# Performance work log

Measured on AMD Instinct MI355X. Metric: run time of the kernel, lower is better.

The kernel has to match this reference:

```python
import jax, jax.numpy as jnp
import numpy as np

NEG = -1e9

def _lstm_dir(x, w_ih, w_hh, b_ih, b_hh):
    # x: (N, T, in) -> (N, T, H); torch gate order i, f, g, o
    xi = x @ w_ih.T + (b_ih + b_hh)  # (N, T, 4H) input projection precomputed
    H = w_hh.shape[1]
    h0 = jnp.zeros((x.shape[0], H), x.dtype)
    def step(carry, xt):
        h, c = carry
        g = xt + h @ w_hh.T
        i, f, gg, o = jnp.split(g, 4, axis=-1)
        c = jax.nn.sigmoid(f) * c + jax.nn.sigmoid(i) * jnp.tanh(gg)
        h = jax.nn.sigmoid(o) * jnp.tanh(c)
        return (h, c), h
    _, ys = jax.lax.scan(step, (h0, h0), jnp.swapaxes(xi, 0, 1))
    return jnp.swapaxes(ys, 0, 1)

def _bilstm_layer(x, wif, whf, bif, bhf, wib, whb, bib, bhb):
    fwd = _lstm_dir(x, wif, whf, bif, bhf)
    bwd = _lstm_dir(x[:, ::-1], wib, whb, bib, bhb)[:, ::-1]
    return jnp.concatenate([fwd, bwd], axis=-1)

def _na1d(x, qkv_w, qkv_b, rpb, proj_w, proj_b, heads, kernel):
    # NATTEN-style 1D neighborhood attention with edge-clamped window + rel pos bias.
    N, L, Dm = x.shape
    hd = Dm // heads
    qkv = x @ qkv_w.T + qkv_b
    q, k, v = jnp.split(qkv, 3, axis=-1)
    sh = lambda t: t.reshape(N, L, heads, hd).transpose(0, 2, 1, 3)
    q, k, v = sh(q) * (hd ** -0.5), sh(k), sh(v)
    scores = jnp.einsum('nhid,nhjd->nhij', q, k)  # (N, heads, L, L)
    i = jnp.arange(L)[:, None]
    j = jnp.arange(L)[None, :]
    start = jnp.clip(i - kernel // 2, 0, L - kernel)     # window start per query
    mask = (j >= start) & (j < start + kernel)           # (L, L) neighborhood mask
    rel = jnp.clip(j - i + kernel - 1, 0, 2 * kernel - 2)
    bias = rpb[:, rel]                                   # (heads, L, L)
    scores = jnp.where(mask, scores + bias, NEG)
    attn = jax.nn.softmax(scores, axis=-1)
    out = jnp.einsum('nhij,nhjd->nhid', attn, v)
    out = out.transpose(0, 2, 1, 3).reshape(N, L, Dm)
    return out @ proj_w.T + proj_b

def setup_inputs() -> dict:
    key = jax.random.key(0)
    ks = iter(jax.random.split(key, 40))
    B, IN, T, P, Dm, H = 4, 256, 256, 88, 128, 64
    p = lambda *s: jax.random.normal(next(ks), s, jnp.float32) * 0.05
    inp = {'x': jax.random.normal(next(ks), (B, IN, T, P), jnp.float32)}
    for l, fin in (('l0', IN), ('l1', Dm)):
        for suf in ('', 'r'):
            inp['w_ih_' + l + suf] = p(4 * H, fin)
            inp['w_hh_' + l + suf] = p(4 * H, H)
            inp['b_ih_' + l + suf] = p(4 * H)
            inp['b_hh_' + l + suf] = p(4 * H)
    for tag, kz in (('t', 7), ('f', 87)):
        inp['qkv_w_' + tag] = p(3 * Dm, Dm)
        inp['qkv_b_' + tag] = p(3 * Dm)
        inp['rpb_' + tag] = p(1, 2 * kz - 1)
        inp['proj_w_' + tag] = p(Dm, Dm)
        inp['proj_b_' + tag] = p(Dm)
    return inp

def reference(x, w_ih_l0, w_hh_l0, b_ih_l0, b_hh_l0, w_ih_l0r, w_hh_l0r, b_ih_l0r, b_hh_l0r, w_ih_l1, w_hh_l1, b_ih_l1, b_hh_l1, w_ih_l1r, w_hh_l1r, b_ih_l1r, b_hh_l1r, qkv_w_t, qkv_b_t, rpb_t, proj_w_t, proj_b_t, qkv_w_f, qkv_b_f, rpb_f, proj_w_f, proj_b_f):
    B, IN, T, P = x.shape
    Dm = proj_w_t.shape[0]
    h = jnp.transpose(x, (0, 3, 2, 1)).reshape(B * P, T, IN)
    h = _bilstm_layer(h, w_ih_l0, w_hh_l0, b_ih_l0, b_hh_l0, w_ih_l0r, w_hh_l0r, b_ih_l0r, b_hh_l0r)
    h = _bilstm_layer(h, w_ih_l1, w_hh_l1, b_ih_l1, b_hh_l1, w_ih_l1r, w_hh_l1r, b_ih_l1r, b_hh_l1r)
    h = _na1d(h, qkv_w_t, qkv_b_t, rpb_t, proj_w_t, proj_b_t, 1, 7)            # time axis
    h = h.reshape(B, P, T, Dm).transpose(0, 2, 1, 3).reshape(B * T, P, Dm)
    h = _na1d(h, qkv_w_f, qkv_b_f, rpb_f, proj_w_f, proj_b_f, 1, 87)           # pitch axis
    return h.reshape(B, T, P, Dm)
```

## Files before the change

### kernel.cpp

```cpp
#include <hip/hip_runtime.h>
#include <cstdint>

#define TP 22528
#define MROWS 90112

typedef __bf16 bf16x8 __attribute__((ext_vector_type(8)));
typedef float  f32x4  __attribute__((ext_vector_type(4)));
typedef unsigned short ushort8 __attribute__((ext_vector_type(8)));

__device__ __forceinline__ unsigned short f2bf(float x) {
    unsigned u = __builtin_bit_cast(unsigned, x);
    return (unsigned short)((u + 0x7fffu + ((u >> 16) & 1u)) >> 16);
}
__device__ __forceinline__ float bf2f(unsigned short h) {
    return __builtin_bit_cast(float, (unsigned)h << 16);
}
__device__ __forceinline__ void gl16(const void* g, void* l) {
    __builtin_amdgcn_global_load_lds(
        (const __attribute__((address_space(1))) void*)g,
        (__attribute__((address_space(3))) void*)l, 16, 0, 0);
}

__global__ void convert_w(const float* __restrict__ s0, const float* __restrict__ s1,
                          const float* __restrict__ s2, const float* __restrict__ s3,
                          const float* __restrict__ s4, const float* __restrict__ s5,
                          const float* __restrict__ s6, const float* __restrict__ s7,
                          unsigned short* __restrict__ WH, unsigned short* __restrict__ WL)
{
    const int stride = gridDim.x * blockDim.x;
    for (int i = blockIdx.x * blockDim.x + threadIdx.x; i < 327680; i += stride) {
        const float* s; int base;
        if      (i <  65536) { s = s0; base = 0; }
        else if (i < 131072) { s = s1; base = 65536; }
        else if (i < 163840) { s = s2; base = 131072; }
        else if (i < 196608) { s = s3; base = 163840; }
        else if (i < 245760) { s = s4; base = 196608; }
        else if (i < 262144) { s = s5; base = 245760; }
        else if (i < 311296) { s = s6; base = 262144; }
        else                 { s = s7; base = 311296; }
        const float v = s[i - base];
        const unsigned short h = f2bf(v);
        WH[i] = h; WL[i] = f2bf(v - bf2f(h));
    }
}

__launch_bounds__(256)
__global__ void transpose_x(const float* __restrict__ x,
                            unsigned short* __restrict__ Xh,
                            unsigned short* __restrict__ Xl)
{
    __shared__ float tile[64][65];
    const int tid = threadIdx.x;
    const int tp0 = blockIdx.x * 64, k0 = blockIdx.y * 64, b = blockIdx.z;
    #pragma unroll
    for (int i = 0; i < 16; ++i) {
        const int idx = i * 256 + tid;
        const int kl = idx >> 6, tpl = idx & 63;
        tile[kl][tpl] = x[(size_t)(b * 256 + k0 + kl) * TP + tp0 + tpl];
    }
    __syncthreads();
    #pragma unroll
    for (int i = 0; i < 2; ++i) {
        const int u = i * 2048 + tid * 8;
        const int ml = u >> 6, kl0 = u & 63;
        ushort8 hi, lo;
        #pragma unroll
        for (int j = 0; j < 8; ++j) {
            const float v = tile[kl0 + j][ml];
            const unsigned short h = f2bf(v);
            hi[j] = h; lo[j] = f2bf(v - bf2f(h));
        }
        const size_t row = (size_t)b * TP + tp0 + ml;
        *(ushort8*)&Xh[row * 256 + k0 + kl0] = hi;
        *(ushort8*)&Xl[row * 256 + k0 + kl0] = lo;
    }
}

template<int OUTBF>
__launch_bounds__(256, 2)
__global__ void gemm_bf16(const unsigned short* __restrict__ Ahi,
                          const unsigned short* __restrict__ Alo,
                          const unsigned short* __restrict__ Whi0,
                          const unsigned short* __restrict__ Wlo0,
                          const unsigned short* __restrict__ Whi1,
                          const unsigned short* __restrict__ Wlo1,
                          const float* __restrict__ b0a, const float* __restrict__ b0b,
                          const float* __restrict__ b1a, const float* __restrict__ b1b,
                          float* __restrict__ C,
                          unsigned short* __restrict__ Chi, unsigned short* __restrict__ Clo,
                          int ldc, int K, int splitN, int NB)
{
    __shared__ unsigned short lds[32768];
    const int tid  = threadIdx.x;
    const int bid  = blockIdx.x;
    const int q8   = (int)gridDim.x >> 3;
    const int wq   = (bid & 7) * q8 + (bid >> 3);
    const int nb   = wq % NB;
    const int mb   = wq / NB;
    const int n0   = nb * 128;
    const int m0   = mb * 128;
    const unsigned short* Wh; const unsigned short* Wl;
    const float* ba; const float* bb; int nr0;
    if (n0 < splitN) { Wh = Whi0; Wl = Wlo0; ba = b0a; bb = b0b; nr0 = n0; }
    else             { Wh = Whi1; Wl = Wlo1; ba = b1a; bb = b1b; nr0 = n0 - splitN; }
    const int lane = tid & 63;
    const int wv   = tid >> 6;
    const int wm   = wv >> 1, wn = wv & 1;
    const int lr   = lane & 15, lg = lane >> 4;
    const int voff = (lane >> 2) * K + (((lane & 3) ^ ((lane >> 2) & 3)) * 8);
    const int wb   = wv * 1024;

    const unsigned short* gAh = Ahi + (size_t)(m0 + wv * 32) * K + voff;
    const unsigned short* gAl = Alo + (size_t)(m0 + wv * 32) * K + voff;
    const unsigned short* gBh = Wh + (size_t)(nr0 + wv * 32) * K + voff;
    const unsigned short* gBl = Wl + (size_t)(nr0 + wv * 32) * K + voff;

    const int NT = K >> 5;
    f32x4 acc[4][4] = {};

    auto stage = [&](int bufi, int ks) {
        unsigned short* base = lds + bufi * 16384;
        gl16(gAh + ks,          base +         wb);
        gl16(gAh + ks + 16 * K, base +         wb + 512);
        gl16(gAl + ks,          base + 4096  + wb);
        gl16(gAl + ks + 16 * K, base + 4096  + wb + 512);
        gl16(gBh + ks,          base + 8192  + wb);
        gl16(gBh + ks + 16 * K, base + 8192  + wb + 512);
        gl16(gBl + ks,          base + 12288 + wb);
        gl16(gBl + ks + 16 * K, base + 12288 + wb + 512);
    };

    stage(0, 0);
    for (int t = 0; t < NT; ++t) {
        const int cur = (t & 1) * 16384;
        if (t + 1 < NT) {
            stage((t & 1) ^ 1, (t + 1) * 32);
            asm volatile("s_waitcnt vmcnt(8)" ::: "memory");
        } else {
            asm volatile("s_waitcnt vmcnt(0)" ::: "memory");
        }
        __builtin_amdgcn_s_barrier();
        __builtin_amdgcn_sched_barrier(0);
        bf16x8 ah[4], al[4], bh[4], bl[4];
        #pragma unroll
        for (int mf = 0; mf < 4; ++mf) {
            const int r = wm * 64 + mf * 16 + lr;
            const int o = r * 32 + ((lg ^ (r & 3)) * 8);
            ah[mf] = *(const bf16x8*)&lds[cur + o];
            al[mf] = *(const bf16x8*)&lds[cur + 4096 + o];
        }
        #pragma unroll
        for (int nf = 0; nf < 4; ++nf) {
            const int r = wn * 64 + nf * 16 + lr;
            const int o = r * 32 + ((lg ^ (r & 3)) * 8);
            bh[nf] = *(const bf16x8*)&lds[cur + 8192 + o];
            bl[nf] = *(const bf16x8*)&lds[cur + 12288 + o];
        }
        #pragma unroll
        for (int mf = 0; mf < 4; ++mf)
            #pragma unroll
            for (int nf = 0; nf < 4; ++nf) {
                acc[mf][nf] = __builtin_amdgcn_mfma_f32_16x16x32_bf16(ah[mf], bh[nf], acc[mf][nf], 0, 0, 0);
                acc[mf][nf] = __builtin_amdgcn_mfma_f32_16x16x32_bf16(ah[mf], bl[nf], acc[mf][nf], 0, 0, 0);
                acc[mf][nf] = __builtin_amdgcn_mfma_f32_16x16x32_bf16(al[mf], bh[nf], acc[mf][nf], 0, 0, 0);
            }
        __builtin_amdgcn_s_barrier();
        __builtin_amdgcn_sched_barrier(0);
    }
    #pragma unroll
    for (int nf = 0; nf < 4; ++nf) {
        const int ncol = wn * 64 + nf * 16 + lr;
        const float bias = ba[nr0 + ncol] + (bb ? bb[nr0 + ncol] : 0.0f);
        #pragma unroll
        for (int mf = 0; mf < 4; ++mf) {
            const int row = m0 + wm * 64 + mf * 16 + lg * 4;
            #pragma unroll
            for (int i = 0; i < 4; ++i) {
                const float v = acc[mf][nf][i] + bias;
                if (OUTBF) {
                    const size_t o = (size_t)(row + i) * ldc + n0 + ncol;
                    const unsigned short h = f2bf(v);
                    Chi[o] = h; Clo[o] = f2bf(v - bf2f(h));
                } else {
                    C[(size_t)(row + i) * ldc + n0 + ncol] = v;
                }
            }
        }
    }
}

__launch_bounds__(256)
__global__ void lstm_kernel(const float* __restrict__ XI,
                            const float* __restrict__ whh_f,
                            const float* __restrict__ whh_b,
                            unsigned short* __restrict__ Hh,
                            unsigned short* __restrict__ Hl)
{
    const int bid = blockIdx.x;
    const int dir = bid & 1;
    const int n   = bid >> 1;
    const int b   = n / 88, p = n - 88 * (n / 88);
    const int j   = threadIdx.x;
    const float* whh = dir ? whh_b : whh_f;
    const int j0 = dir ? 256 : 0;
    const int ho = dir ? 64 : 0;
    float w[64];
    #pragma unroll
    for (int k = 0; k < 64; k += 4) {
        const float4 wv = *(const float4*)(whh + (size_t)j * 64 + k);
        w[k] = wv.x; w[k+1] = wv.y; w[k+2] = wv.z; w[k+3] = wv.w;
    }
    __shared__ float h_sh[64];
    __shared__ float acts[256];
    if (j < 64) h_sh[j] = 0.0f;
    float c = 0.0f;
    __syncthreads();
    const size_t rowbase = (size_t)(b * 256) * 88 + p;
    float pref = XI[(rowbase + (size_t)(dir ? 255 : 0) * 88) * 512 + j0 + j];
    for (int step = 0; step < 256; ++step) {
        const int t = dir ? (255 - step) : step;
        const size_t r = rowbase + (size_t)t * 88;
        float gs0 = pref, gs1 = 0.0f, gs2 = 0.0f, gs3 = 0.0f;
        if (step + 1 < 256) {
            const int tn = dir ? (254 - step) : (step + 1);
            pref = XI[(rowbase + (size_t)tn * 88) * 512 + j0 + j];
        }
        #pragma unroll
        for (int k = 0; k < 64; k += 16) {
            const float4 h0 = *(const float4*)&h_sh[k];
            const float4 h1 = *(const float4*)&h_sh[k + 4];
            const float4 h2 = *(const float4*)&h_sh[k + 8];
            const float4 h3 = *(const float4*)&h_sh[k + 12];
            gs0 += h0.x * w[k]    + h0.y * w[k+1]  + h0.z * w[k+2]  + h0.w * w[k+3];
            gs1 += h1.x * w[k+4]  + h1.y * w[k+5]  + h1.z * w[k+6]  + h1.w * w[k+7];
            gs2 += h2.x * w[k+8]  + h2.y * w[k+9]  + h2.z * w[k+10] + h2.w * w[k+11];
            gs3 += h3.x * w[k+12] + h3.y * w[k+13] + h3.z * w[k+14] + h3.w * w[k+15];
        }
        const float g = (gs0 + gs1) + (gs2 + gs3);
        float a;
        if (j >= 128 && j < 192) {
            const float e = __expf(2.0f * g);
            a = 1.0f - 2.0f / (e + 1.0f);
        } else {
            a = 1.0f / (1.0f + __expf(-g));
        }
        acts[j] = a;
        __syncthreads();
        if (j < 64) {
            const float ai = acts[j], af = acts[64 + j], ag = acts[128 + j], ao = acts[192 + j];
            c = af * c + ai * ag;
            const float e = __expf(2.0f * c);
            const float th = 1.0f - 2.0f / (e + 1.0f);
            const float h = ao * th;
            h_sh[j] = h;
            const size_t o = r * 128 + ho + j;
            const unsigned short hh = f2bf(h);
            Hh[o] = hh; Hl[o] = f2bf(h - bf2f(hh));
        }
        __syncthreads();
    }
}

__launch_bounds__(256)
__global__ void na_t_kernel(const float* __restrict__ QKV,
                            const float* __restrict__ rpb,
                            unsigned short* __restrict__ OUTh,
                            unsigned short* __restrict__ OUTl)
{
    const int wave = threadIdx.x >> 6;
    const int lane = threadIdx.x & 63;
    const int q = blockIdx.x * 4 + wave;
    const int b = q / TP; int rem = q - b * TP;
    const int i = rem / 88; const int p = rem - 88 * (rem / 88);
    int start = i - 3; if (start < 0) start = 0; if (start > 249) start = 249;
    const float scale = 0.08838834764831845f;
    const float* qrow = QKV + (size_t)q * 384;
    const float q0 = qrow[lane] * scale;
    const float q1 = qrow[lane + 64] * scale;
    const size_t rbase = (size_t)(b * 256) * 88 + p;
    float s[7];
    #pragma unroll
    for (int jj = 0; jj < 7; ++jj) {
        const int t = start + jj;
        const float* krow = QKV + (rbase + (size_t)t * 88) * 384 + 128;
        float part = q0 * krow[lane] + q1 * krow[lane + 64];
        part += __shfl_xor(part, 1);
        part += __shfl_xor(part, 2);
        part += __shfl_xor(part, 4);
        part += __shfl_xor(part, 8);
        part += __shfl_xor(part, 16);
        part += __shfl_xor(part, 32);
        int rel = t - i + 6; if (rel < 0) rel = 0; if (rel > 12) rel = 12;
        s[jj] = part + rpb[rel];
    }
    float m = s[0];
    #pragma unroll
    for (int jj = 1; jj < 7; ++jj) m = fmaxf(m, s[jj]);
    float sum = 0.0f;
    #pragma unroll
    for (int jj = 0; jj < 7; ++jj) { s[jj] = __expf(s[jj] - m); sum += s[jj]; }
    const float inv = 1.0f / sum;
    float o0 = 0.0f, o1 = 0.0f;
    #pragma unroll
    for (int jj = 0; jj < 7; ++jj) {
        const float* vrow = QKV + (rbase + (size_t)(start + jj) * 88) * 384 + 256;
        const float pj = s[jj] * inv;
        o0 += pj * vrow[lane];
        o1 += pj * vrow[lane + 64];
    }
    const size_t oi = (size_t)q * 128 + lane;
    const unsigned short h0 = f2bf(o0);
    OUTh[oi] = h0; OUTl[oi] = f2bf(o0 - bf2f(h0));
    const unsigned short h1 = f2bf(o1);
    OUTh[oi + 64] = h1; OUTl[oi + 64] = f2bf(o1 - bf2f(h1));
}

#define LPAD 133
#define SPAD 89
__launch_bounds__(256)
__global__ void na_f_kernel(const float* __restrict__ QKV,
                            const float* __restrict__ rpb,
                            unsigned short* __restrict__ OUTh,
                            unsigned short* __restrict__ OUTl)
{
    __shared__ float Qs[96][LPAD];
    __shared__ float Ks[96][LPAD];
    __shared__ float Ss[96][SPAD];
    const int blk = blockIdx.x;
    const int tid = threadIdx.x;
    const size_t base = (size_t)blk * 88 * 384;
    const float scale = 0.08838834764831845f;
    for (int f = tid; f < 2816; f += 256) {
        const int row = f >> 5, c4 = (f & 31) * 4;
        const float4 qv = *(const float4*)(QKV + base + (size_t)row * 384 + c4);
        Qs[row][c4+0] = qv.x * scale; Qs[row][c4+1] = qv.y * scale;
        Qs[row][c4+2] = qv.z * scale; Qs[row][c4+3] = qv.w * scale;
        const float4 kv = *(const float4*)(QKV + base + (size_t)row * 384 + 128 + c4);
        Ks[row][c4+0] = kv.x; Ks[row][c4+1] = kv.y;
        Ks[row][c4+2] = kv.z; Ks[row][c4+3] = kv.w;
    }
    __syncthreads();
    const int tx = tid & 15, ty = tid >> 4;
    {
        float acc[6][6] = {};
        for (int kk = 0; kk < 128; ++kk) {
            float a[6], bb[6];
            #pragma unroll
            for (int i = 0; i < 6; ++i) a[i] = Qs[ty*6 + i][kk];
            #pragma unroll
            for (int j = 0; j < 6; ++j) bb[j] = Ks[tx*6 + j][kk];
            #pragma unroll
            for (int i = 0; i < 6; ++i)
                #pragma unroll
                for (int j = 0; j < 6; ++j)
                    acc[i][j] += a[i] * bb[j];
        }
        #pragma unroll
        for (int i = 0; i < 6; ++i) {
            const int qq = ty*6 + i;
            if (qq < 88) {
                #pragma unroll
                for (int j = 0; j < 6; ++j) {
                    const int k = tx*6 + j;
                    if (k < 88) Ss[qq][k] = acc[i][j];
                }
            }
        }
    }
    __syncthreads();
    for (int f = tid; f < 2816; f += 256) {
        const int row = f >> 5, c4 = (f & 31) * 4;
        const float4 vv = *(const float4*)(QKV + base + (size_t)row * 384 + 256 + c4);
        Ks[row][c4+0] = vv.x; Ks[row][c4+1] = vv.y;
        Ks[row][c4+2] = vv.z; Ks[row][c4+3] = vv.w;
    }
    if (tid < 88) {
        const int i = tid;
        const int jex = (i <= 43) ? 87 : 0;
        float m = -1e30f;
        for (int k = 0; k < 88; ++k) {
            if (k == jex) continue;
            int rel = k - i + 86; if (rel < 0) rel = 0; if (rel > 172) rel = 172;
            const float v = Ss[i][k] + rpb[rel];
            Ss[i][k] = v;
            m = fmaxf(m, v);
        }
        float sum = 0.0f;
        for (int k = 0; k < 88; ++k) {
            if (k == jex) continue;
            const float e = __expf(Ss[i][k] - m);
            Ss[i][k] = e;
            sum += e;
        }
        const float inv = 1.0f / sum;
        for (int k = 0; k < 88; ++k) Ss[i][k] = (k == jex) ? 0.0f : Ss[i][k] * inv;
    }
    __syncthreads();
    {
        float o[6][8] = {};
        for (int k = 0; k < 88; ++k) {
            float pv[6], vv[8];
            #pragma unroll
            for (int i = 0; i < 6; ++i) pv[i] = Ss[ty*6 + i][k];
            #pragma unroll
            for (int j = 0; j < 8; ++j) vv[j] = Ks[k][tx + 16*j];
            #pragma unroll
            for (int i = 0; i < 6; ++i)
                #pragma unroll
                for (int j = 0; j < 8; ++j)
                    o[i][j] += pv[i] * vv[j];
        }
        #pragma unroll
        for (int i = 0; i < 6; ++i) {
            const int qq = ty*6 + i;
            if (qq < 88) {
                const size_t ro = ((size_t)blk * 88 + qq) * 128;
                #pragma unroll
                for (int j = 0; j < 8; ++j) {
                    const float v = o[i][j];
                    const unsigned short hh = f2bf(v);
                    OUTh[ro + tx + 16*j] = hh;
                    OUTl[ro + tx + 16*j] = f2bf(v - bf2f(hh));
                }
            }
        }
    }
}

extern "C" void kernel_launch(void* const* d_in, const int* in_sizes, int n_in,
                              void* d_out, int out_size, void* d_ws, size_t ws_size,
                              hipStream_t stream)
{
    const float* x         = (const float*)d_in[0];
    const float* w_ih_l0   = (const float*)d_in[1];
    const float* w_hh_l0   = (const float*)d_in[2];
    const float* b_ih_l0   = (const float*)d_in[3];
    const float* b_hh_l0   = (const float*)d_in[4];
    const float* w_ih_l0r  = (const float*)d_in[5];
    const float* w_hh_l0r  = (const float*)d_in[6];
    const float* b_ih_l0r  = (const float*)d_in[7];
    const float* b_hh_l0r  = (const float*)d_in[8];
    const float* w_ih_l1   = (const float*)d_in[9];
    const float* w_hh_l1   = (const float*)d_in[10];
    const float* b_ih_l1   = (const float*)d_in[11];
    const float* b_hh_l1   = (const float*)d_in[12];
    const float* w_ih_l1r  = (const float*)d_in[13];
    const float* w_hh_l1r  = (const float*)d_in[14];
    const float* b_ih_l1r  = (const float*)d_in[15];
    const float* b_hh_l1r  = (const float*)d_in[16];
    const float* qkv_w_t   = (const float*)d_in[17];
    const float* qkv_b_t   = (const float*)d_in[18];
    const float* rpb_t     = (const float*)d_in[19];
    const float* proj_w_t  = (const float*)d_in[20];
    const float* proj_b_t  = (const float*)d_in[21];
    const float* qkv_w_f   = (const float*)d_in[22];
    const float* qkv_b_f   = (const float*)d_in[23];
    const float* rpb_f     = (const float*)d_in[24];
    const float* proj_w_f  = (const float*)d_in[25];
    const float* proj_b_f  = (const float*)d_in[26];

    float* ws = (float*)d_ws;
    float*          XI   = ws;
    float*          QKV  = ws;
    unsigned short* ATTh = (unsigned short*)(ws + (size_t)MROWS * 384);
    unsigned short* ATTl = ATTh + (size_t)MROWS * 128;
    unsigned short* Hh   = (unsigned short*)(ws + 46137344);
    unsigned short* Hl   = Hh + (size_t)MROWS * 128;
    unsigned short* Gh   = (unsigned short*)(ws + 57671680);
    unsigned short* Gl   = Gh + (size_t)MROWS * 128;
    unsigned short* Xh   = (unsigned short*)(ws + 46137344);
    unsigned short* Xl   = Xh + (size_t)MROWS * 256;
    unsigned short* WH   = (unsigned short*)(ws + 69206016);
    unsigned short* WL   = WH + 327680;

    const int BIG = 1 << 30;
    const dim3 blk(256);

    convert_w<<<dim3(320), blk, 0, stream>>>(w_ih_l0, w_ih_l0r, w_ih_l1, w_ih_l1r,
        qkv_w_t, proj_w_t, qkv_w_f, proj_w_f, WH, WL);
    transpose_x<<<dim3(352, 4, 4), blk, 0, stream>>>(x, Xh, Xl);
    gemm_bf16<0><<<dim3(2816), blk, 0, stream>>>(Xh, Xl,
        WH, WL, WH + 65536, WL + 65536,
        b_ih_l0, b_hh_l0, b_ih_l0r, b_hh_l0r,
        XI, nullptr, nullptr, 512, 256, 256, 4);
    lstm_kernel<<<dim3(704), blk, 0, stream>>>(XI, w_hh_l0, w_hh_l0r, Hh, Hl);
    gemm_bf16<0><<<dim3(2816), blk, 0, stream>>>(Hh, Hl,
        WH + 131072, WL + 131072, WH + 163840, WL + 163840,
        b_ih_l1, b_hh_l1, b_ih_l1r, b_hh_l1r,
        XI, nullptr, nullptr, 512, 128, 256, 4);
    lstm_kernel<<<dim3(704), blk, 0, stream>>>(XI, w_hh_l1, w_hh_l1r, Hh, Hl);
    gemm_bf16<0><<<dim3(2112), blk, 0, stream>>>(Hh, Hl,
        WH + 196608, WL + 196608, WH + 196608, WL + 196608,
        qkv_b_t, nullptr, qkv_b_t, nullptr,
        QKV, nullptr, nullptr, 384, 128, BIG, 3);
    na_t_kernel<<<dim3(22528), blk, 0, stream>>>(QKV, rpb_t, ATTh, ATTl);
    gemm_bf16<1><<<dim3(704), blk, 0, stream>>>(ATTh, ATTl,
        WH + 245760, WL + 245760, WH + 245760, WL + 245760,
        proj_b_t, nullptr, proj_b_t, nullptr,
        nullptr, Gh, Gl, 128, 128, BIG, 1);
    gemm_bf16<0><<<dim3(2112), blk, 0, stream>>>(Gh, Gl,
        WH + 262144, WL + 262144, WH + 262144, WL + 262144,
        qkv_b_f, nullptr, qkv_b_f, nullptr,
        QKV, nullptr, nullptr, 384, 128, BIG, 3);
    na_f_kernel<<<dim3(1024), blk, 0, stream>>>(QKV, rpb_f, ATTh, ATTl);
    gemm_bf16<0><<<dim3(704), blk, 0, stream>>>(ATTh, ATTl,
        WH + 311296, WL + 311296, WH + 311296, WL + 311296,
        proj_b_f, nullptr, proj_b_f, nullptr,
        (float*)d_out, nullptr, nullptr, 128, 128, BIG, 1);
}
```

Before: 1.104 ms.

## Halve LSTM block to 128 threads, each computing two gates in registers

The recurrent LSTM kernel now uses 128 threads per sequence instead of 256. Each thread holds two rows of W_hh: wave 0 computes the i and g gates, wave 1 the f and o gates. Only the i*g product goes through shared memory, so the 256-entry activation array is dropped. This roughly halves the threads waiting at each per-timestep barrier and removes most of the shared-memory traffic on the serial critical path. In exchange, register use per thread doubles to 128 weight floats and each thread does twice the FMA work per step.

```diff
diff --git a/kernel.cpp b/kernel.cpp
--- a/kernel.cpp
+++ b/kernel.cpp
@@ -189,7 +189,7 @@
     }
 }
 
-__launch_bounds__(256)
+__launch_bounds__(128)
 __global__ void lstm_kernel(const float* __restrict__ XI,
                             const float* __restrict__ whh_f,
                             const float* __restrict__ whh_b,
@@ -200,60 +200,69 @@
     const int dir = bid & 1;
     const int n   = bid >> 1;
     const int b   = n / 88, p = n - 88 * (n / 88);
-    const int j   = threadIdx.x;
+    const int tid = threadIdx.x;
+    const int u   = tid & 63;
+    const int wv  = tid >> 6;
     const float* whh = dir ? whh_b : whh_f;
     const int j0 = dir ? 256 : 0;
     const int ho = dir ? 64 : 0;
-    float w[64];
+    const int rowA = wv * 64 + u;
+    const int rowB = 128 + wv * 64 + u;
+    float wA[64], wB[64];
     #pragma unroll
     for (int k = 0; k < 64; k += 4) {
-        const float4 wv = *(const float4*)(whh + (size_t)j * 64 + k);
-        w[k] = wv.x; w[k+1] = wv.y; w[k+2] = wv.z; w[k+3] = wv.w;
+        const float4 wa = *(const float4*)(whh + (size_t)rowA * 64 + k);
+        wA[k] = wa.x; wA[k+1] = wa.y; wA[k+2] = wa.z; wA[k+3] = wa.w;
+        const float4 wb2 = *(const float4*)(whh + (size_t)rowB * 64 + k);
+        wB[k] = wb2.x; wB[k+1] = wb2.y; wB[k+2] = wb2.z; wB[k+3] = wb2.w;
     }
     __shared__ float h_sh[64];
-    __shared__ float acts[256];
-    if (j < 64) h_sh[j] = 0.0f;
+    __shared__ float ig_sh[64];
+    if (tid < 64) h_sh[tid] = 0.0f;
     float c = 0.0f;
     __syncthreads();
     const size_t rowbase = (size_t)(b * 256) * 88 + p;
-    float pref = XI[(rowbase + (size_t)(dir ? 255 : 0) * 88) * 512 + j0 + j];
+    const size_t r0 = rowbase + (size_t)(dir ? 255 : 0) * 88;
+    float prefA = XI[r0 * 512 + j0 + rowA];
+    float prefB = XI[r0 * 512 + j0 + rowB];
     for (int step = 0; step < 256; ++step) {
         const int t = dir ? (255 - step) : step;
         const size_t r = rowbase + (size_t)t * 88;
-        float gs0 = pref, gs1 = 0.0f, gs2 = 0.0f, gs3 = 0.0f;
+        float gA0 = prefA, gA1 = 0.0f, gB0 = prefB, gB1 = 0.0f;
         if (step + 1 < 256) {
             const int tn = dir ? (254 - step) : (step + 1);
-            pref = XI[(rowbase + (size_t)tn * 88) * 512 + j0 + j];
-        }
-        #pragma unroll
-        for (int k = 0; k < 64; k += 16) {
+            const size_t rn = rowbase + (size_t)tn * 88;
+            prefA = XI[rn * 512 + j0 + rowA];
+            prefB = XI[rn * 512 + j0 + rowB];
+        }
+        #pragma unroll
+        for (int k = 0; k < 64; k += 8) {
             const float4 h0 = *(const float4*)&h_sh[k];
             const float4 h1 = *(const float4*)&h_sh[k + 4];
-            const float4 h2 = *(const float4*)&h_sh[k + 8];
-            const float4 h3 = *(const float4*)&h_sh[k + 12];
-            gs0 += h0.x * w[k]    + h0.y * w[k+1]  + h0.z * w[k+2]  + h0.w * w[k+3];
-            gs1 += h1.x * w[k+4]  + h1.y * w[k+5]  + h1.z * w[k+6]  + h1.w * w[k+7];
-            gs2 += h2.x * w[k+8]  + h2.y * w[k+9]  + h2.z * w[k+10] + h2.w * w[k+11];
-            gs3 += h3.x * w[k+12] + h3.y * w[k+13] + h3.z * w[k+14] + h3.w * w[k+15];
-        }
-        const float g = (gs0 + gs1) + (gs2 + gs3);
-        float a;
-        if (j >= 128 && j < 192) {
-            const float e = __expf(2.0f * g);
-            a = 1.0f - 2.0f / (e + 1.0f);
+            gA0 += h0.x * wA[k]   + h0.y * wA[k+1] + h0.z * wA[k+2] + h0.w * wA[k+3];
+            gA1 += h1.x * wA[k+4] + h1.y * wA[k+5] + h1.z * wA[k+6] + h1.w * wA[k+7];
+            gB0 += h0.x * wB[k]   + h0.y * wB[k+1] + h0.z * wB[k+2] + h0.w * wB[k+3];
+            gB1 += h1.x * wB[k+4] + h1.y * wB[k+5] + h1.z * wB[k+6] + h1.w * wB[k+7];
+        }
+        const float gAs = gA0 + gA1;
+        const float gBs = gB0 + gB1;
+        const float aA = 1.0f / (1.0f + __expf(-gAs));
+        float aB;
+        if (wv == 0) {
+            const float e = __expf(2.0f * gBs);
+            aB = 1.0f - 2.0f / (e + 1.0f);
         } else {
-            a = 1.0f / (1.0f + __expf(-g));
-        }
-        acts[j] = a;
+            aB = 1.0f / (1.0f + __expf(-gBs));
+        }
+        if (wv == 0) ig_sh[u] = aA * aB;
         __syncthreads();
-        if (j < 64) {
-            const float ai = acts[j], af = acts[64 + j], ag = acts[128 + j], ao = acts[192 + j];
-            c = af * c + ai * ag;
+        if (wv == 1) {
+            c = aA * c + ig_sh[u];
             const float e = __expf(2.0f * c);
             const float th = 1.0f - 2.0f / (e + 1.0f);
-            const float h = ao * th;
-            h_sh[j] = h;
-            const size_t o = r * 128 + ho + j;
+            const float h = aB * th;
+            h_sh[u] = h;
+            const size_t o = r * 128 + ho + u;
             const unsigned short hh = f2bf(h);
             Hh[o] = hh; Hl[o] = f2bf(h - bf2f(hh));
         }
@@ -483,12 +492,12 @@
         WH, WL, WH + 65536, WL + 65536,
         b_ih_l0, b_hh_l0, b_ih_l0r, b_hh_l0r,
         XI, nullptr, nullptr, 512, 256, 256, 4);
-    lstm_kernel<<<dim3(704), blk, 0, stream>>>(XI, w_hh_l0, w_hh_l0r, Hh, Hl);
+    lstm_kernel<<<dim3(704), dim3(128), 0, stream>>>(XI, w_hh_l0, w_hh_l0r, Hh, Hl);
     gemm_bf16<0><<<dim3(2816), blk, 0, stream>>>(Hh, Hl,
         WH + 131072, WL + 131072, WH + 163840, WL + 163840,
         b_ih_l1, b_hh_l1, b_ih_l1r, b_hh_l1r,
         XI, nullptr, nullptr, 512, 128, 256, 4);
-    lstm_kernel<<<dim3(704), blk, 0, stream>>>(XI, w_hh_l1, w_hh_l1r, Hh, Hl);
+    lstm_kernel<<<dim3(704), dim3(128), 0, stream>>>(XI, w_hh_l1, w_hh_l1r, Hh, Hl);
     gemm_bf16<0><<<dim3(2112), blk, 0, stream>>>(Hh, Hl,
         WH + 196608, WL + 196608, WH + 196608, WL + 196608,
         qkv_b_t, nullptr, qkv_b_t, nullptr,
```

New measurement: 1.172 ms. 6.2% more time.
